# Kernel optimization log

Hardware: AMD Instinct MI355X
Metric: run time of the kernel (lower is better)

The kernel has to match this reference:

```python
import jax, jax.numpy as jnp
import numpy as np

NUM_HEADS = 8
NUM_POINTS = 4


def _bilinear(img, xs, ys):
    """Bilinear sample with zero padding (grid_sample align_corners=False).
    img: [N, H, W, C]; xs, ys: [N, P] pixel-space coords. Returns [N, P, C]."""
    H, W = img.shape[1], img.shape[2]
    x0 = jnp.floor(xs)
    y0 = jnp.floor(ys)
    wx = xs - x0
    wy = ys - y0
    x0i = x0.astype(jnp.int32)
    y0i = y0.astype(jnp.int32)

    def g(ix, iy):
        valid = ((ix >= 0) & (ix < W) & (iy >= 0) & (iy < H)).astype(img.dtype)
        ixc = jnp.clip(ix, 0, W - 1)
        iyc = jnp.clip(iy, 0, H - 1)
        v = jax.vmap(lambda im, yy, xx: im[yy, xx])(img, iyc, ixc)  # [N,P,C]
        return v * valid[..., None]

    return (g(x0i, y0i) * ((1 - wx) * (1 - wy))[..., None]
            + g(x0i + 1, y0i) * (wx * (1 - wy))[..., None]
            + g(x0i, y0i + 1) * ((1 - wx) * wy)[..., None]
            + g(x0i + 1, y0i + 1) * (wx * wy)[..., None])


def setup_inputs() -> dict:
    key = jax.random.key(0)
    ks = jax.random.split(key, 10)
    BN, C, H, W = 12, 256, 40, 100
    nq = H * W
    hp = NUM_HEADS * NUM_POINTS
    s = 1.0 / np.sqrt(C).astype(np.float32)
    return {
        "img_feats": jax.random.normal(ks[0], (BN, C, H, W), jnp.float32),
        "warp_grid": jax.random.uniform(ks[1], (BN, H, W, 2), jnp.float32),
        "reference_points": jax.random.uniform(ks[2], (BN, nq, 1, 2), jnp.float32),
        "Wv": jax.random.normal(ks[3], (C, C), jnp.float32) * s,
        "bv": jnp.zeros((C,), jnp.float32),
        "Woff": jax.random.normal(ks[4], (C, hp * 2), jnp.float32) * 0.01,
        "boff": jax.random.normal(ks[5], (hp * 2,), jnp.float32) * 0.5,
        "Wattn": jax.random.normal(ks[6], (C, hp), jnp.float32) * 0.01,
        "battn": jnp.zeros((hp,), jnp.float32),
        "Wout": jax.random.normal(ks[7], (C, C), jnp.float32) * s,
        "bout": jnp.zeros((C,), jnp.float32),
    }


def reference(img_feats, warp_grid, reference_points,
              Wv, bv, Woff, boff, Wattn, battn, Wout, bout):
    BN, C, H, W = img_feats.shape
    heads, pts = NUM_HEADS, NUM_POINTS
    hd = C // heads
    nq = H * W

    feat = img_feats.transpose(0, 2, 3, 1)  # [BN, H, W, C]

    # BEVWarp: bilinear warp of image features at the projected grid ([0,1] normed)
    gx = warp_grid[..., 0].reshape(BN, -1) * W - 0.5
    gy = warp_grid[..., 1].reshape(BN, -1) * H - 0.5
    warped = _bilinear(feat, gx, gy)          # [BN, nq, C] -> value
    query = feat.reshape(BN, nq, C)           # flattened img feats -> query

    # MultiScaleDeformableAttention, num_levels=1
    v = (warped @ Wv + bv).reshape(BN, nq, heads, hd)
    off = (query @ Woff + boff).reshape(BN, nq, heads, pts, 2)
    attn = jax.nn.softmax((query @ Wattn + battn).reshape(BN, nq, heads, pts), axis=-1)

    norm = jnp.array([W, H], dtype=img_feats.dtype)
    loc = reference_points.reshape(BN, nq, 1, 1, 2) + off / norm  # [BN,nq,h,p,2]

    vh = v.transpose(0, 2, 1, 3).reshape(BN * heads, H, W, hd)
    lx = (loc[..., 0] * W - 0.5).transpose(0, 2, 1, 3).reshape(BN * heads, nq * pts)
    ly = (loc[..., 1] * H - 0.5).transpose(0, 2, 1, 3).reshape(BN * heads, nq * pts)
    sampled = _bilinear(vh, lx, ly).reshape(BN, heads, nq, pts, hd)

    agg = jnp.einsum('bhqpd,bqhp->bqhd', sampled, attn).reshape(BN, nq, C)
    out = agg @ Wout + bout + query  # output_proj + residual (dropout=0 at eval)
    return out.transpose(0, 2, 1).reshape(BN, C, H, W)
```

## Files before the change

### kernel.cpp

```cpp
#include <hip/hip_runtime.h>

#define DEVINL __device__ __forceinline__

typedef __attribute__((ext_vector_type(4))) float f32x4;
typedef __attribute__((ext_vector_type(8))) short short8;

constexpr int kBN = 12, kC = 256, kH = 40, kW = 100;
constexpr int kNQ = kH * kW;
constexpr int kM = kBN * kNQ;

DEVINL float bflo(uint p) { union { uint i; float f; } v; v.i = p << 16; return v.f; }
DEVINL float bfhi(uint p) { union { uint i; float f; } v; v.i = p & 0xffff0000u; return v.f; }
DEVINL ushort f2bf(float f) {
  union { float f; uint i; } v; v.f = f;
  uint i = v.i;
  return (ushort)((i + 0x7fffu + ((i >> 16) & 1u)) >> 16);
}
DEVINL uint pack2(float a, float b) { return (uint)f2bf(a) | ((uint)f2bf(b) << 16); }

DEVINL void mfma_bf16(f32x4& acc, short8 a, short8 b) {
  acc = __builtin_amdgcn_mfma_f32_16x16x32_bf16(a, b, acc, 0, 0, 0);
}

DEVINL void gload16(const ushort* g, char* lds) {
  __builtin_amdgcn_global_load_lds(
      (const __attribute__((address_space(1))) uint*)g,
      (__attribute__((address_space(3))) uint*)lds, 16, 0, 0);
}

DEVINL void acc8(float* acc, uint4 d, float wv) {
  acc[0] += wv * bflo(d.x); acc[1] += wv * bfhi(d.x);
  acc[2] += wv * bflo(d.y); acc[3] += wv * bfhi(d.y);
  acc[4] += wv * bflo(d.z); acc[5] += wv * bfhi(d.z);
  acc[6] += wv * bflo(d.w); acc[7] += wv * bfhi(d.w);
}

__global__ __launch_bounds__(256) void k_wt_all(const float* __restrict__ Wv,
                                                const float* __restrict__ Woff,
                                                const float* __restrict__ Wattn,
                                                const float* __restrict__ Wout,
                                                ushort* __restrict__ WvT,
                                                ushort* __restrict__ WoffT,
                                                ushort* __restrict__ WattnT,
                                                ushort* __restrict__ WoutT) {
  int idx = blockIdx.x * 256 + threadIdx.x;
  const float* W; ushort* WT; int N, base;
  if (idx < 65536)       { W = Wv;    WT = WvT;    N = 256; base = 0; }
  else if (idx < 81920)  { W = Woff;  WT = WoffT;  N = 64;  base = 65536; }
  else if (idx < 90112)  { W = Wattn; WT = WattnT; N = 32;  base = 81920; }
  else if (idx < 155648) { W = Wout;  WT = WoutT;  N = 256; base = 90112; }
  else return;
  int i = idx - base;
  int n = i >> 8, k = i & 255;
  WT[i] = f2bf(W[k * N + n]);
}

__global__ __launch_bounds__(256) void k_transpose(const float* __restrict__ img,
                                                   ushort* __restrict__ feat) {
  __shared__ ushort tile[64][66];
  int b = blockIdx.z, c0 = blockIdx.y * 64, q0 = blockIdx.x * 64;
  int t = threadIdx.x;
  int ql = t & 63, cl = t >> 6;
#pragma unroll
  for (int i = 0; i < 16; ++i) {
    int c = cl + i * 4, q = q0 + ql;
    float v = (q < kNQ) ? img[(size_t)(b * kC + c0 + c) * kNQ + q] : 0.f;
    tile[c][ql] = f2bf(v);
  }
  __syncthreads();
  int cc = t & 63, qr = t >> 6;
#pragma unroll
  for (int i = 0; i < 16; ++i) {
    int qlo = qr + i * 4, q = q0 + qlo;
    if (q < kNQ) feat[(size_t)(b * kNQ + q) * kC + c0 + cc] = tile[cc][qlo];
  }
}

__global__ __launch_bounds__(256) void k_warp(const ushort* __restrict__ feat,
                                              const float* __restrict__ grid,
                                              ushort* __restrict__ warped) {
  int orig = blockIdx.x;
  int n = (orig & 7) * 750 + (orig >> 3);
  int t = threadIdx.x;
  int ql = t >> 5, g = t & 31;
  int gq = n * 8 + ql;
  int b = gq / kNQ;
  float gx = grid[(size_t)gq * 2 + 0] * kW - 0.5f;
  float gy = grid[(size_t)gq * 2 + 1] * kH - 0.5f;
  float x0f = floorf(gx), y0f = floorf(gy);
  int x0 = (int)x0f, y0 = (int)y0f;
  float wx = gx - x0f, wy = gy - y0f;
  float acc[8];
#pragma unroll
  for (int i = 0; i < 8; ++i) acc[i] = 0.f;
  const ushort* fb = feat + (size_t)b * kNQ * kC + g * 8;
#pragma unroll
  for (int ty = 0; ty < 2; ++ty) {
    int iy = y0 + ty;
    if (iy < 0 || iy >= kH) continue;
    float wyv = ty ? wy : 1.f - wy;
#pragma unroll
    for (int tx = 0; tx < 2; ++tx) {
      int ix = x0 + tx;
      if (ix < 0 || ix >= kW) continue;
      float wv = wyv * (tx ? wx : 1.f - wx);
      uint4 d = *(const uint4*)(fb + (size_t)(iy * kW + ix) * kC);
      acc8(acc, d, wv);
    }
  }
  uint o[4] = {pack2(acc[0], acc[1]), pack2(acc[2], acc[3]),
               pack2(acc[4], acc[5]), pack2(acc[6], acc[7])};
  *(uint4*)(warped + (size_t)gq * kC + g * 8) = *(uint4*)o;
}

template <int EPI>
__global__ __launch_bounds__(256) void k_gemm256(const ushort* __restrict__ A,
                                                 const ushort* __restrict__ BT,
                                                 const float* __restrict__ bias,
                                                 ushort* __restrict__ Obf,
                                                 float* __restrict__ Ofp,
                                                 const float* __restrict__ resid) {
  extern __shared__ char smem[];
  const int t = threadIdx.x, wave = t >> 6, lane = t & 63;
  const int l15 = lane & 15, l4 = lane >> 4;
  const int b = blockIdx.x / 63, mb = blockIdx.x % 63;
  const int q0 = mb * 64;
  const int nrows = (kNQ - q0 < 64) ? (kNQ - q0) : 64;
  const int n0w = wave * 64;
  const int ra = t >> 2, ca = t & 3;
  const int rac = (ra < nrows) ? ra : (nrows - 1);
  const int sca = ca ^ ((ra >> 1) & 3);
  const ushort* gA = A + ((size_t)b * kNQ + q0 + rac) * 256 + sca * 8;
  const ushort* gB = BT + (size_t)ra * 256 + sca * 8;

  f32x4 acc[4][4];
#pragma unroll
  for (int i = 0; i < 4; ++i)
#pragma unroll
    for (int j = 0; j < 4; ++j) acc[i][j] = (f32x4)0.f;

  auto STAGE = [&](int buf, int kk) {
    char* Asb = smem + buf * 20480;
    char* Bsb = Asb + 4096;
    gload16(gA + kk, Asb + t * 16);
#pragma unroll
    for (int i = 0; i < 4; ++i)
      gload16(gB + (size_t)i * 64 * 256 + kk, Bsb + (i * 256 + t) * 16);
  };

  STAGE(0, 0);
  int cur = 0;
#pragma unroll 1
  for (int step = 0; step < 8; ++step) {
    if (step < 7) {
      STAGE(cur ^ 1, (step + 1) * 32);
      asm volatile("s_waitcnt vmcnt(5)" ::: "memory");
    } else {
      asm volatile("s_waitcnt vmcnt(0)" ::: "memory");
    }
    __builtin_amdgcn_s_barrier();
    asm volatile("" ::: "memory");
    char* Asb = smem + cur * 20480;
    char* Bsb = Asb + 4096;
    short8 af[4], bf[4];
#pragma unroll
    for (int mf = 0; mf < 4; ++mf) {
      int r = mf * 16 + l15;
      int sl = l4 ^ ((r >> 1) & 3);
      af[mf] = *(const short8*)(Asb + r * 64 + sl * 16);
    }
#pragma unroll
    for (int nf = 0; nf < 4; ++nf) {
      int r = n0w + nf * 16 + l15;
      int sl = l4 ^ ((r >> 1) & 3);
      bf[nf] = *(const short8*)(Bsb + r * 64 + sl * 16);
    }
#pragma unroll
    for (int mf = 0; mf < 4; ++mf)
#pragma unroll
      for (int nf = 0; nf < 4; ++nf) mfma_bf16(acc[mf][nf], af[mf], bf[nf]);
    asm volatile("" ::: "memory");
    __builtin_amdgcn_s_barrier();
    cur ^= 1;
  }

  if (EPI == 0) {
#pragma unroll
    for (int mf = 0; mf < 4; ++mf) {
      if (mf * 16 >= nrows) continue;
      int q = q0 + mf * 16 + l4 * 4;
#pragma unroll
      for (int nf = 0; nf < 4; ++nf) {
        int col = n0w + nf * 16 + l15;
        float bv = bias[col];
        int h = col >> 5, ch = col & 31;
        ushort* dst = Obf + (size_t)(b * 8 + h) * kNQ * 32 + ch;
#pragma unroll
        for (int j = 0; j < 4; ++j)
          dst[(size_t)(q + j) * 32] = f2bf(acc[mf][nf][j] + bv);
      }
    }
  } else {
    float* Tw = (float*)(smem + wave * 4352);
#pragma unroll
    for (int nf = 0; nf < 4; ++nf) {
      float bv = bias[n0w + nf * 16 + l15];
#pragma unroll
      for (int mf = 0; mf < 4; ++mf)
#pragma unroll
        for (int j = 0; j < 4; ++j)
          Tw[l15 * 68 + mf * 16 + l4 * 4 + j] = acc[mf][nf][j] + bv;
      int c = l15, rs = l4 * 16;
      if (rs < nrows) {
        int col = n0w + nf * 16 + c;
        size_t gi = ((size_t)b * kC + col) * kNQ + q0 + rs;
#pragma unroll
        for (int k = 0; k < 4; ++k) {
          float4 tv = *(float4*)(&Tw[c * 68 + rs + k * 4]);
          float4 rv = *(const float4*)(resid + gi + k * 4);
          tv.x += rv.x; tv.y += rv.y; tv.z += rv.z; tv.w += rv.w;
          *(float4*)(Ofp + gi + k * 4) = tv;
        }
      }
    }
  }
}

__global__ __launch_bounds__(256) void k_offattn(const ushort* __restrict__ A,
                                                 const ushort* __restrict__ WoffT,
                                                 const ushort* __restrict__ WattnT,
                                                 const float* __restrict__ boff,
                                                 const float* __restrict__ battn,
                                                 const float* __restrict__ refp,
                                                 float* __restrict__ samp) {
  extern __shared__ char smem[];
  float* T = (float*)smem;
  const int t = threadIdx.x, wave = t >> 6, lane = t & 63;
  const int l15 = lane & 15, l4 = lane >> 4;
  const int b = blockIdx.x / 63, mb = blockIdx.x % 63;
  const int q0 = mb * 64;
  const int nrows = (kNQ - q0 < 64) ? (kNQ - q0) : 64;
  const int wr = wave >> 1, wc = wave & 1;
  const int ra = t >> 2, ca = t & 3;
  const int sca = ca ^ ((ra >> 1) & 3);
  const ushort* gA  = A + ((size_t)b * kNQ + q0 + ra) * 256 + sca * 8;
  const ushort* gB0 = WoffT + (size_t)ra * 256 + sca * 8;
  const ushort* gB1 = WattnT + (size_t)ra * 256 + sca * 8;
  const bool doA = (ra < nrows);

  f32x4 acc[2][3];
#pragma unroll
  for (int i = 0; i < 2; ++i)
#pragma unroll
    for (int j = 0; j < 3; ++j) acc[i][j] = (f32x4)0.f;

  auto STAGE = [&](int buf, int kk) {
    char* Asb = smem + buf * 10240;
    char* Bsb = Asb + 4096;
    if (doA) gload16(gA + kk, Asb + t * 16);
    gload16(gB0 + kk, Bsb + t * 16);
    if (t < 128) gload16(gB1 + kk, Bsb + (256 + t) * 16);
  };

  STAGE(0, 0);
  __syncthreads();
  int cur = 0;
#pragma unroll 1
  for (int step = 0; step < 8; ++step) {
    if (step < 7) STAGE(cur ^ 1, (step + 1) * 32);
    char* Asb = smem + cur * 10240;
    char* Bsb = Asb + 4096;
    short8 af[2], bf[3];
#pragma unroll
    for (int mf = 0; mf < 2; ++mf) {
      int r = wr * 32 + mf * 16 + l15;
      int sl = l4 ^ ((r >> 1) & 3);
      af[mf] = *(const short8*)(Asb + r * 64 + sl * 16);
    }
#pragma unroll
    for (int nf = 0; nf < 3; ++nf) {
      int r = wc * 48 + nf * 16 + l15;
      int sl = l4 ^ ((r >> 1) & 3);
      bf[nf] = *(const short8*)(Bsb + r * 64 + sl * 16);
    }
#pragma unroll
    for (int mf = 0; mf < 2; ++mf)
#pragma unroll
      for (int nf = 0; nf < 3; ++nf) mfma_bf16(acc[mf][nf], af[mf], bf[nf]);
    __syncthreads();
    cur ^= 1;
  }

#pragma unroll
  for (int nf = 0; nf < 3; ++nf) {
    int col = wc * 48 + nf * 16 + l15;
    float bv = (col < 64) ? boff[col] : battn[col - 64];
#pragma unroll
    for (int mf = 0; mf < 2; ++mf)
#pragma unroll
      for (int j = 0; j < 4; ++j) {
        int row = wr * 32 + mf * 16 + l4 * 4 + j;
        T[row * 101 + col] = acc[mf][nf][j] + bv;
      }
  }
  __syncthreads();
  int row = t >> 2;
  if (row < nrows) {
    int q = q0 + row;
    float refx = refp[((size_t)b * kNQ + q) * 2 + 0] * kW - 0.5f;
    float refy = refp[((size_t)b * kNQ + q) * 2 + 1] * kH - 0.5f;
#pragma unroll
    for (int hi2 = 0; hi2 < 2; ++hi2) {
      int h = (t & 3) + hi2 * 4;
      float sx[4], sy[4], lg[4];
#pragma unroll
      for (int p = 0; p < 4; ++p) {
        sx[p] = refx + T[row * 101 + h * 8 + p * 2 + 0];
        sy[p] = refy + T[row * 101 + h * 8 + p * 2 + 1];
        lg[p] = T[row * 101 + 64 + h * 4 + p];
      }
      float mx = fmaxf(fmaxf(lg[0], lg[1]), fmaxf(lg[2], lg[3]));
      float e[4], s = 0.f;
#pragma unroll
      for (int p = 0; p < 4; ++p) { e[p] = __expf(lg[p] - mx); s += e[p]; }
      float inv = 1.f / s;
      float* dst = samp + (((size_t)(b * 8 + h) * kNQ + q) * 4) * 3;
#pragma unroll
      for (int p = 0; p < 4; ++p) {
        dst[p * 3 + 0] = sx[p];
        dst[p * 3 + 1] = sy[p];
        dst[p * 3 + 2] = e[p] * inv;
      }
    }
  }
}

__global__ __launch_bounds__(256) void k_sample(const ushort* __restrict__ v,
                                                const float* __restrict__ samp,
                                                ushort* __restrict__ agg) {
  int orig = blockIdx.x;
  int n = (orig & 7) * 756 + (orig >> 3);
  int plane = n / 63, chunk = n - plane * 63;
  int t = threadIdx.x;
  int ql = t >> 2, g = t & 3;
  int q = chunk * 64 + ql;
  if (q >= kNQ) return;
  int b = plane >> 3, h = plane & 7;
  const ushort* pv = v + (size_t)plane * kNQ * 32 + g * 8;
  const int lane = t & 63, gbase = lane & ~3;

  const float* sp = samp + (((size_t)plane * kNQ + q) * 4 + g) * 3;
  float myx = sp[0], myy = sp[1], myw = sp[2];
  float acc[8];
#pragma unroll
  for (int i = 0; i < 8; ++i) acc[i] = 0.f;
#pragma unroll
  for (int p = 0; p < 4; ++p) {
    float sxp = __shfl(myx, gbase + p);
    float syp = __shfl(myy, gbase + p);
    float wp  = __shfl(myw, gbase + p);
    float x0f = floorf(sxp), y0f = floorf(syp);
    int x0 = (int)x0f, y0 = (int)y0f;
    float wx = sxp - x0f, wy = syp - y0f;
#pragma unroll
    for (int ty = 0; ty < 2; ++ty) {
      int iy = y0 + ty;
      if (iy < 0 || iy >= kH) continue;
      float wyv = ty ? wy : 1.f - wy;
#pragma unroll
      for (int tx = 0; tx < 2; ++tx) {
        int ix = x0 + tx;
        if (ix < 0 || ix >= kW) continue;
        float wv = wp * wyv * (tx ? wx : 1.f - wx);
        uint4 d = *(const uint4*)(pv + (size_t)(iy * kW + ix) * 32);
        acc8(acc, d, wv);
      }
    }
  }
  uint o[4] = {pack2(acc[0], acc[1]), pack2(acc[2], acc[3]),
               pack2(acc[4], acc[5]), pack2(acc[6], acc[7])};
  *(uint4*)(agg + ((size_t)b * kNQ + q) * kC + h * 32 + g * 8) = *(uint4*)o;
}

extern "C" void kernel_launch(void* const* d_in, const int* in_sizes, int n_in,
                              void* d_out, int out_size, void* d_ws, size_t ws_size,
                              hipStream_t stream) {
  const float* img   = (const float*)d_in[0];
  const float* grid  = (const float*)d_in[1];
  const float* refp  = (const float*)d_in[2];
  const float* Wv    = (const float*)d_in[3];
  const float* bv    = (const float*)d_in[4];
  const float* Woff  = (const float*)d_in[5];
  const float* boff  = (const float*)d_in[6];
  const float* Wattn = (const float*)d_in[7];
  const float* battn = (const float*)d_in[8];
  const float* Wout  = (const float*)d_in[9];
  const float* bout  = (const float*)d_in[10];
  float* out = (float*)d_out;

  char* ws = (char*)d_ws;
  const size_t SZ = (size_t)kM * kC * 2;
  ushort* feat   = (ushort*)(ws);
  ushort* warped = (ushort*)(ws + SZ);
  ushort* vbuf   = (ushort*)(ws + 2 * SZ);
  float*  samp   = (float*)(ws + 3 * SZ);
  ushort* WvT    = (ushort*)(ws + 4 * SZ);
  ushort* WoffT  = (ushort*)(ws + 4 * SZ + 131072);
  ushort* WattnT = (ushort*)(ws + 4 * SZ + 131072 + 32768);
  ushort* WoutT  = (ushort*)(ws + 4 * SZ + 131072 + 32768 + 16384);
  ushort* aggb   = warped;

  k_wt_all<<<608, 256, 0, stream>>>(Wv, Woff, Wattn, Wout, WvT, WoffT, WattnT, WoutT);
  k_transpose<<<dim3(63, 4, 12), 256, 0, stream>>>(img, feat);
  k_warp<<<6000, 256, 0, stream>>>(feat, grid, warped);
  k_gemm256<0><<<756, 256, 40960, stream>>>(warped, WvT, bv, vbuf, nullptr, nullptr);
  k_offattn<<<756, 256, 25856, stream>>>(feat, WoffT, WattnT, boff, battn, refp, samp);
  k_sample<<<6048, 256, 0, stream>>>(vbuf, samp, aggb);
  k_gemm256<1><<<756, 256, 40960, stream>>>(aggb, WoutT, bout, nullptr, out, img);
}
```

Before: 123.4 us.

## Fuse bilinear warp into value-projection GEMM via LDS-resident A tile

Removes the separate warp kernel by having each GEMM block bilinearly sample its 64 query rows directly into a full 64x256 swizzled A tile in LDS, then running the K loop with only the weight operand double-buffered from global memory. This cuts a kernel launch and the global write and re-read of the warped intermediate. In exchange, LDS per block grows to 64 KB, which may lower occupancy, and the gather latency is no longer overlapped with MFMA work inside the block. Block indices are also remapped to group work per XCD.

```diff
diff --git a/kernel.cpp b/kernel.cpp
--- a/kernel.cpp
+++ b/kernel.cpp
@@ -76,48 +76,135 @@
   }
 }
 
-__global__ __launch_bounds__(256) void k_warp(const ushort* __restrict__ feat,
-                                              const float* __restrict__ grid,
-                                              ushort* __restrict__ warped) {
+__global__ __launch_bounds__(256) void k_gemmv_fused(const ushort* __restrict__ feat,
+                                                     const float* __restrict__ grid,
+                                                     const ushort* __restrict__ BT,
+                                                     const float* __restrict__ bias,
+                                                     ushort* __restrict__ Obf) {
+  extern __shared__ char smem[];
+  char* Afull = smem;
+  const int t = threadIdx.x, wave = t >> 6, lane = t & 63;
+  const int l15 = lane & 15, l4 = lane >> 4;
+
   int orig = blockIdx.x;
-  int n = (orig & 7) * 750 + (orig >> 3);
-  int t = threadIdx.x;
-  int ql = t >> 5, g = t & 31;
-  int gq = n * 8 + ql;
-  int b = gq / kNQ;
-  float gx = grid[(size_t)gq * 2 + 0] * kW - 0.5f;
-  float gy = grid[(size_t)gq * 2 + 1] * kH - 0.5f;
-  float x0f = floorf(gx), y0f = floorf(gy);
-  int x0 = (int)x0f, y0 = (int)y0f;
-  float wx = gx - x0f, wy = gy - y0f;
-  float acc[8];
-#pragma unroll
-  for (int i = 0; i < 8; ++i) acc[i] = 0.f;
-  const ushort* fb = feat + (size_t)b * kNQ * kC + g * 8;
-#pragma unroll
-  for (int ty = 0; ty < 2; ++ty) {
-    int iy = y0 + ty;
-    if (iy < 0 || iy >= kH) continue;
-    float wyv = ty ? wy : 1.f - wy;
-#pragma unroll
-    for (int tx = 0; tx < 2; ++tx) {
-      int ix = x0 + tx;
-      if (ix < 0 || ix >= kW) continue;
-      float wv = wyv * (tx ? wx : 1.f - wx);
-      uint4 d = *(const uint4*)(fb + (size_t)(iy * kW + ix) * kC);
-      acc8(acc, d, wv);
-    }
-  }
-  uint o[4] = {pack2(acc[0], acc[1]), pack2(acc[2], acc[3]),
-               pack2(acc[4], acc[5]), pack2(acc[6], acc[7])};
-  *(uint4*)(warped + (size_t)gq * kC + g * 8) = *(uint4*)o;
-}
-
-template <int EPI>
-__global__ __launch_bounds__(256) void k_gemm256(const ushort* __restrict__ A,
+  int xcd = orig % 8, ii = orig / 8;
+  int n = (xcd < 4 ? xcd * 95 : 380 + (xcd - 4) * 94) + ii;
+  const int b = n / 63, mb = n % 63;
+  const int q0 = mb * 64;
+  const int nrows = (kNQ - q0 < 64) ? (kNQ - q0) : 64;
+  const int n0w = wave * 64;
+
+  {
+    const int g = t & 31;
+    const int qa = t >> 5;
+    const ushort* fb = feat + (size_t)b * kNQ * kC + g * 8;
+#pragma unroll 1
+    for (int pass = 0; pass < 8; ++pass) {
+      int ql = pass * 8 + qa;
+      int qlc = (ql < nrows) ? ql : (nrows - 1);
+      size_t gq = (size_t)b * kNQ + q0 + qlc;
+      float gx = grid[gq * 2 + 0] * kW - 0.5f;
+      float gy = grid[gq * 2 + 1] * kH - 0.5f;
+      float x0f = floorf(gx), y0f = floorf(gy);
+      int x0 = (int)x0f, y0 = (int)y0f;
+      float wx = gx - x0f, wy = gy - y0f;
+      float acc[8];
+#pragma unroll
+      for (int i = 0; i < 8; ++i) acc[i] = 0.f;
+#pragma unroll
+      for (int ty = 0; ty < 2; ++ty) {
+        int iy = y0 + ty;
+        if (iy < 0 || iy >= kH) continue;
+        float wyv = ty ? wy : 1.f - wy;
+#pragma unroll
+        for (int tx = 0; tx < 2; ++tx) {
+          int ix = x0 + tx;
+          if (ix < 0 || ix >= kW) continue;
+          float wv = wyv * (tx ? wx : 1.f - wx);
+          uint4 d = *(const uint4*)(fb + (size_t)(iy * kW + ix) * kC);
+          acc8(acc, d, wv);
+        }
+      }
+      uint o[4] = {pack2(acc[0], acc[1]), pack2(acc[2], acc[3]),
+                   pack2(acc[4], acc[5]), pack2(acc[6], acc[7])};
+      int sslot = (g & 3) ^ ((ql >> 1) & 3);
+      *(uint4*)(Afull + ql * 512 + (g >> 2) * 64 + sslot * 16) = *(uint4*)o;
+    }
+  }
+  __syncthreads();
+
+  const int ra = t >> 2, ca = t & 3;
+  const int sca = ca ^ ((ra >> 1) & 3);
+  const ushort* gB = BT + (size_t)ra * 256 + sca * 8;
+
+  f32x4 acc[4][4];
+#pragma unroll
+  for (int i = 0; i < 4; ++i)
+#pragma unroll
+    for (int j = 0; j < 4; ++j) acc[i][j] = (f32x4)0.f;
+
+  auto STAGE_B = [&](int buf, int kk) {
+    char* Bsb = smem + 32768 + buf * 16384;
+#pragma unroll
+    for (int i = 0; i < 4; ++i)
+      gload16(gB + (size_t)i * 64 * 256 + kk, Bsb + (i * 256 + t) * 16);
+  };
+
+  STAGE_B(0, 0);
+  int cur = 0;
+#pragma unroll 1
+  for (int step = 0; step < 8; ++step) {
+    if (step < 7) {
+      STAGE_B(cur ^ 1, (step + 1) * 32);
+      asm volatile("s_waitcnt vmcnt(4)" ::: "memory");
+    } else {
+      asm volatile("s_waitcnt vmcnt(0)" ::: "memory");
+    }
+    __builtin_amdgcn_s_barrier();
+    asm volatile("" ::: "memory");
+    char* Bsb = smem + 32768 + cur * 16384;
+    short8 af[4], bf[4];
+#pragma unroll
+    for (int mf = 0; mf < 4; ++mf) {
+      int r = mf * 16 + l15;
+      int sl = l4 ^ ((r >> 1) & 3);
+      af[mf] = *(const short8*)(Afull + r * 512 + step * 64 + sl * 16);
+    }
+#pragma unroll
+    for (int nf = 0; nf < 4; ++nf) {
+      int r = n0w + nf * 16 + l15;
+      int sl = l4 ^ ((r >> 1) & 3);
+      bf[nf] = *(const short8*)(Bsb + r * 64 + sl * 16);
+    }
+#pragma unroll
+    for (int mf = 0; mf < 4; ++mf)
+#pragma unroll
+      for (int nf = 0; nf < 4; ++nf) mfma_bf16(acc[mf][nf], af[mf], bf[nf]);
+    asm volatile("" ::: "memory");
+    __builtin_amdgcn_s_barrier();
+    cur ^= 1;
+  }
+
+#pragma unroll
+  for (int mf = 0; mf < 4; ++mf) {
+    if (mf * 16 >= nrows) continue;
+    int q = q0 + mf * 16 + l4 * 4;
+#pragma unroll
+    for (int nf = 0; nf < 4; ++nf) {
+      int col = n0w + nf * 16 + l15;
+      float bv = bias[col];
+      int h = col >> 5, ch = col & 31;
+      ushort* dst = Obf + (size_t)(b * 8 + h) * kNQ * 32 + ch;
+#pragma unroll
+      for (int j = 0; j < 4; ++j)
+        dst[(size_t)(q + j) * 32] = f2bf(acc[mf][nf][j] + bv);
+    }
+  }
+}
+
+__global__ __launch_bounds__(256) void k_gemmout(const ushort* __restrict__ A,
                                                  const ushort* __restrict__ BT,
                                                  const float* __restrict__ bias,
-                                                 ushort* __restrict__ Obf,
                                                  float* __restrict__ Ofp,
                                                  const float* __restrict__ resid) {
   extern __shared__ char smem[];
@@ -184,43 +271,25 @@
     cur ^= 1;
   }
 
-  if (EPI == 0) {
-#pragma unroll
-    for (int mf = 0; mf < 4; ++mf) {
-      if (mf * 16 >= nrows) continue;
-      int q = q0 + mf * 16 + l4 * 4;
-#pragma unroll
-      for (int nf = 0; nf < 4; ++nf) {
-        int col = n0w + nf * 16 + l15;
-        float bv = bias[col];
-        int h = col >> 5, ch = col & 31;
-        ushort* dst = Obf + (size_t)(b * 8 + h) * kNQ * 32 + ch;
-#pragma unroll
-        for (int j = 0; j < 4; ++j)
-          dst[(size_t)(q + j) * 32] = f2bf(acc[mf][nf][j] + bv);
-      }
-    }
-  } else {
-    float* Tw = (float*)(smem + wave * 4352);
-#pragma unroll
-    for (int nf = 0; nf < 4; ++nf) {
-      float bv = bias[n0w + nf * 16 + l15];
-#pragma unroll
-      for (int mf = 0; mf < 4; ++mf)
-#pragma unroll
-        for (int j = 0; j < 4; ++j)
-          Tw[l15 * 68 + mf * 16 + l4 * 4 + j] = acc[mf][nf][j] + bv;
-      int c = l15, rs = l4 * 16;
-      if (rs < nrows) {
-        int col = n0w + nf * 16 + c;
-        size_t gi = ((size_t)b * kC + col) * kNQ + q0 + rs;
-#pragma unroll
-        for (int k = 0; k < 4; ++k) {
-          float4 tv = *(float4*)(&Tw[c * 68 + rs + k * 4]);
-          float4 rv = *(const float4*)(resid + gi + k * 4);
-          tv.x += rv.x; tv.y += rv.y; tv.z += rv.z; tv.w += rv.w;
-          *(float4*)(Ofp + gi + k * 4) = tv;
-        }
+  float* Tw = (float*)(smem + wave * 4352);
+#pragma unroll
+  for (int nf = 0; nf < 4; ++nf) {
+    float bv = bias[n0w + nf * 16 + l15];
+#pragma unroll
+    for (int mf = 0; mf < 4; ++mf)
+#pragma unroll
+      for (int j = 0; j < 4; ++j)
+        Tw[l15 * 68 + mf * 16 + l4 * 4 + j] = acc[mf][nf][j] + bv;
+    int c = l15, rs = l4 * 16;
+    if (rs < nrows) {
+      int col = n0w + nf * 16 + c;
+      size_t gi = ((size_t)b * kC + col) * kNQ + q0 + rs;
+#pragma unroll
+      for (int k = 0; k < 4; ++k) {
+        float4 tv = *(float4*)(&Tw[c * 68 + rs + k * 4]);
+        float4 rv = *(const float4*)(resid + gi + k * 4);
+        tv.x += rv.x; tv.y += rv.y; tv.z += rv.z; tv.w += rv.w;
+        *(float4*)(Ofp + gi + k * 4) = tv;
       }
     }
   }
@@ -401,20 +470,18 @@
   char* ws = (char*)d_ws;
   const size_t SZ = (size_t)kM * kC * 2;
   ushort* feat   = (ushort*)(ws);
-  ushort* warped = (ushort*)(ws + SZ);
+  ushort* aggb   = (ushort*)(ws + SZ);
   ushort* vbuf   = (ushort*)(ws + 2 * SZ);
   float*  samp   = (float*)(ws + 3 * SZ);
   ushort* WvT    = (ushort*)(ws + 4 * SZ);
   ushort* WoffT  = (ushort*)(ws + 4 * SZ + 131072);
   ushort* WattnT = (ushort*)(ws + 4 * SZ + 131072 + 32768);
   ushort* WoutT  = (ushort*)(ws + 4 * SZ + 131072 + 32768 + 16384);
-  ushort* aggb   = warped;
 
   k_wt_all<<<608, 256, 0, stream>>>(Wv, Woff, Wattn, Wout, WvT, WoffT, WattnT, WoutT);
   k_transpose<<<dim3(63, 4, 12), 256, 0, stream>>>(img, feat);
-  k_warp<<<6000, 256, 0, stream>>>(feat, grid, warped);
-  k_gemm256<0><<<756, 256, 40960, stream>>>(warped, WvT, bv, vbuf, nullptr, nullptr);
+  k_gemmv_fused<<<756, 256, 65536, stream>>>(feat, grid, WvT, bv, vbuf);
   k_offattn<<<756, 256, 25856, stream>>>(feat, WoffT, WattnT, boff, battn, refp, samp);
   k_sample<<<6048, 256, 0, stream>>>(vbuf, samp, aggb);
-  k_gemm256<1><<<756, 256, 40960, stream>>>(aggb, WoutT, bout, nullptr, out, img);
-}
+  k_gemmout<<<756, 256, 40960, stream>>>(aggb, WoutT, bout, out, img);
+}
```

Measured after the change: 136.4 us. 10.5% more time.

## Vectorize transpose stores and pipeline offattn GEMM loads with partial vmcnt waits

Applied to the files above, without the earlier changes.

The transpose kernel now writes 16-byte vectors of eight channels per thread instead of scalar 2-byte stores, which cuts the number of global store transactions. In k_offattn the A-row loads are clamped to the last valid row rather than predicated, so every wave issues the same number of async loads. The __syncthreads calls become explicit s_waitcnt vmcnt(N) plus raw s_barrier, so the next stage's prefetch can stay in flight while the current tile is consumed. The wait counts are hand-tuned to the per-wave load count and are fragile if the compiler reorders or adds memory ops.

```diff
diff --git a/kernel.cpp b/kernel.cpp
--- a/kernel.cpp
+++ b/kernel.cpp
@@ -68,11 +68,17 @@
     tile[c][ql] = f2bf(v);
   }
   __syncthreads();
-  int cc = t & 63, qr = t >> 6;
-#pragma unroll
-  for (int i = 0; i < 16; ++i) {
-    int qlo = qr + i * 4, q = q0 + qlo;
-    if (q < kNQ) feat[(size_t)(b * kNQ + q) * kC + c0 + cc] = tile[cc][qlo];
+#pragma unroll
+  for (int i = 0; i < 2; ++i) {
+    int idx = t + i * 256;
+    int qlo = idx >> 3, cg = idx & 7;
+    int q = q0 + qlo;
+    if (q < kNQ) {
+      ushort tmp[8];
+#pragma unroll
+      for (int j = 0; j < 8; ++j) tmp[j] = tile[cg * 8 + j][qlo];
+      *(uint4*)(feat + ((size_t)b * kNQ + q) * kC + c0 + cg * 8) = *(uint4*)tmp;
+    }
   }
 }
 
@@ -242,11 +248,11 @@
   const int nrows = (kNQ - q0 < 64) ? (kNQ - q0) : 64;
   const int wr = wave >> 1, wc = wave & 1;
   const int ra = t >> 2, ca = t & 3;
+  const int rac = (ra < nrows) ? ra : (nrows - 1);
   const int sca = ca ^ ((ra >> 1) & 3);
-  const ushort* gA  = A + ((size_t)b * kNQ + q0 + ra) * 256 + sca * 8;
+  const ushort* gA  = A + ((size_t)b * kNQ + q0 + rac) * 256 + sca * 8;
   const ushort* gB0 = WoffT + (size_t)ra * 256 + sca * 8;
   const ushort* gB1 = WattnT + (size_t)ra * 256 + sca * 8;
-  const bool doA = (ra < nrows);
 
   f32x4 acc[2][3];
 #pragma unroll
@@ -257,17 +263,24 @@
   auto STAGE = [&](int buf, int kk) {
     char* Asb = smem + buf * 10240;
     char* Bsb = Asb + 4096;
-    if (doA) gload16(gA + kk, Asb + t * 16);
+    gload16(gA + kk, Asb + t * 16);
     gload16(gB0 + kk, Bsb + t * 16);
     if (t < 128) gload16(gB1 + kk, Bsb + (256 + t) * 16);
   };
 
   STAGE(0, 0);
-  __syncthreads();
   int cur = 0;
 #pragma unroll 1
   for (int step = 0; step < 8; ++step) {
-    if (step < 7) STAGE(cur ^ 1, (step + 1) * 32);
+    if (step < 7) {
+      STAGE(cur ^ 1, (step + 1) * 32);
+      if (wave < 2) asm volatile("s_waitcnt vmcnt(3)" ::: "memory");
+      else          asm volatile("s_waitcnt vmcnt(2)" ::: "memory");
+    } else {
+      asm volatile("s_waitcnt vmcnt(0)" ::: "memory");
+    }
+    __builtin_amdgcn_s_barrier();
+    asm volatile("" ::: "memory");
     char* Asb = smem + cur * 10240;
     char* Bsb = Asb + 4096;
     short8 af[2], bf[3];
@@ -287,7 +300,8 @@
     for (int mf = 0; mf < 2; ++mf)
 #pragma unroll
       for (int nf = 0; nf < 3; ++nf) mfma_bf16(acc[mf][nf], af[mf], bf[nf]);
-    __syncthreads();
+    asm volatile("" ::: "memory");
+    __builtin_amdgcn_s_barrier();
     cur ^= 1;
   }
 
```

Measured after the change: 122.6 us. About the same (-0.7%).
